# Kernel tuning notes

Measured on AMD Instinct MI355X. Metric: run time of the kernel, lower is better.

The kernel has to match this reference:

```python
import jax, jax.numpy as jnp
import numpy as np

B, L, D = 4, 4096, 1024
LN_EPS = 1e-5
SCAN_EPS = 1e-8


def setup_inputs() -> dict:
    key = jax.random.key(0)
    ks = jax.random.split(key, 5)
    s = 1.0 / np.sqrt(D)
    return {
        "X": jax.random.normal(ks[0], (B, L, D), dtype=jnp.float32),
        "Wa": jax.random.normal(ks[1], (D, D), dtype=jnp.float32) * s,
        "ba": jnp.zeros((D,), dtype=jnp.float32),
        "Wb": jax.random.normal(ks[2], (D, D), dtype=jnp.float32) * s,
        "bb": jnp.zeros((D,), dtype=jnp.float32),
        "Wc": jax.random.normal(ks[3], (D, D), dtype=jnp.float32) * s,
        "bc": jnp.zeros((D,), dtype=jnp.float32),
        "gamma": jnp.ones((D,), dtype=jnp.float32),
        "beta": jnp.zeros((D,), dtype=jnp.float32),
        "h0": jax.random.normal(ks[4], (1, D), dtype=jnp.float32),
    }


def reference(X, Wa, ba, Wb, bb, Wc, bc, gamma, beta, h0):
    # LayerNorm over last dim
    mu = jnp.mean(X, axis=-1, keepdims=True)
    var = jnp.mean(jnp.square(X - mu), axis=-1, keepdims=True)
    Z = (X - mu) * jax.lax.rsqrt(var + LN_EPS) * gamma + beta  # [B,L,D]

    A = jax.nn.sigmoid(jnp.einsum("bld,ed->ble", Z, Wa) + ba)   # gate in (0,1)
    P = jnp.cumprod(A, axis=1)                                   # decay products
    Bx = jnp.einsum("bld,ed->ble", Z, Wb) + bb
    S = jnp.cumsum(Bx / (P + SCAN_EPS), axis=1)
    # h_t = P_t * h0 + P_t * sum_{s<=t} Bx_s / P_s   (linear recurrence)
    h = P * (h0[:, None, :] + S)                                 # h0 [1,D] broadcasts
    C = jnp.einsum("bld,ed->ble", Z, Wc) + bc
    return C * h + X  # dropout is identity at inference
```

## Files before the change

kernel.cpp:

```cpp
#include <hip/hip_runtime.h>
#include <hip/hip_bf16.h>
#include <cstdint>
#include <cstddef>

#define B_ 4
#define L_ 4096
#define D_ 1024
#define M_ (B_ * L_)
#define LN_EPS 1e-5f
#define SCAN_EPS 1e-8f
#define CT 64
#define NC (L_ / CT)

typedef float f32x4 __attribute__((ext_vector_type(4)));
typedef short bf16x8 __attribute__((ext_vector_type(8)));

__device__ __forceinline__ void gload_lds16(const void* g, void* l) {
    __builtin_amdgcn_global_load_lds(
        (const __attribute__((address_space(1))) void*)g,
        (__attribute__((address_space(3))) void*)l, 16, 0, 0);
}

__global__ __launch_bounds__(256) void ln_kernel(
    const float* __restrict__ X, const float* __restrict__ gamma,
    const float* __restrict__ beta, __hip_bfloat16* __restrict__ Zb)
{
    const int row = blockIdx.x;
    const int tid = threadIdx.x;
    const float* x = X + (size_t)row * D_;

    float4 v = *reinterpret_cast<const float4*>(x + tid * 4);
    float s = v.x + v.y + v.z + v.w;
    #pragma unroll
    for (int off = 32; off > 0; off >>= 1) s += __shfl_down(s, off);

    __shared__ float red[4];
    __shared__ float red2[4];
    const int wid = tid >> 6, lane = tid & 63;
    if (lane == 0) red[wid] = s;
    __syncthreads();
    const float mean = (red[0] + red[1] + red[2] + red[3]) * (1.0f / D_);

    const float dx = v.x - mean, dy = v.y - mean, dz = v.z - mean, dw = v.w - mean;
    float s2 = dx * dx + dy * dy + dz * dz + dw * dw;
    #pragma unroll
    for (int off = 32; off > 0; off >>= 1) s2 += __shfl_down(s2, off);
    if (lane == 0) red2[wid] = s2;
    __syncthreads();
    const float var = (red2[0] + red2[1] + red2[2] + red2[3]) * (1.0f / D_);
    const float rs = rsqrtf(var + LN_EPS);

    float4 g  = *reinterpret_cast<const float4*>(gamma + tid * 4);
    float4 be = *reinterpret_cast<const float4*>(beta + tid * 4);
    union { ushort4 u4; __hip_bfloat16 h[4]; } pk;
    pk.h[0] = __float2bfloat16(dx * rs * g.x + be.x);
    pk.h[1] = __float2bfloat16(dy * rs * g.y + be.y);
    pk.h[2] = __float2bfloat16(dz * rs * g.z + be.z);
    pk.h[3] = __float2bfloat16(dw * rs * g.w + be.w);
    *reinterpret_cast<ushort4*>(Zb + (size_t)row * D_ + tid * 4) = pk.u4;
}

__global__ __launch_bounds__(256) void cvt_w3(
    const float* __restrict__ Wa, const float* __restrict__ Wb,
    const float* __restrict__ Wc, __hip_bfloat16* __restrict__ Wbf)
{
    const int gid = blockIdx.x * 256 + threadIdx.x;
    const size_t i = (size_t)gid * 8;
    const int which = (int)(i >> 20);
    const size_t off = i & ((1ull << 20) - 1);
    const float* W = (which == 0) ? Wa : (which == 1) ? Wb : Wc;
    float4 v0 = *reinterpret_cast<const float4*>(W + off);
    float4 v1 = *reinterpret_cast<const float4*>(W + off + 4);
    union { bf16x8 v; __hip_bfloat16 h[8]; } pk;
    pk.h[0] = __float2bfloat16(v0.x); pk.h[1] = __float2bfloat16(v0.y);
    pk.h[2] = __float2bfloat16(v0.z); pk.h[3] = __float2bfloat16(v0.w);
    pk.h[4] = __float2bfloat16(v1.x); pk.h[5] = __float2bfloat16(v1.y);
    pk.h[6] = __float2bfloat16(v1.z); pk.h[7] = __float2bfloat16(v1.w);
    *reinterpret_cast<bf16x8*>(Wbf + i) = pk.v;
}

#define TM 128
#define TN 128
#define TK 32

__global__ __launch_bounds__(256) void gemm3_mfma(
    const __hip_bfloat16* __restrict__ Zb, const __hip_bfloat16* __restrict__ Wbf,
    const float* __restrict__ ba, const float* __restrict__ bb, const float* __restrict__ bc,
    float* __restrict__ Aout, float* __restrict__ Bxout, float* __restrict__ Cout)
{
    __shared__ __hip_bfloat16 As[TM * TK];
    __shared__ __hip_bfloat16 Bs[TN * TK];

    const int tid  = threadIdx.x;
    const int wv   = tid >> 6;
    const int lane = tid & 63;
    const int wr   = wv >> 1, wc = wv & 1;
    const int m0   = blockIdx.y * TM;
    const int n0g  = blockIdx.x * TN;
    const int which = n0g >> 10;
    const int n0   = n0g & 1023;

    const __hip_bfloat16* __restrict__ Wsrc = Wbf + ((size_t)which << 20);
    const float* __restrict__ bias = (which == 0) ? ba : (which == 1) ? bb : bc;

    const int c0 = tid, c1 = 256 + tid;
    const int row0 = c0 >> 2, sc0 = (c0 & 3) ^ ((row0 >> 1) & 3);
    const int row1 = c1 >> 2, sc1 = (c1 & 3) ^ ((row1 >> 1) & 3);
    __hip_bfloat16* aDst0 = As + (size_t)(wv * 64) * 8;
    __hip_bfloat16* aDst1 = As + (size_t)(256 + wv * 64) * 8;
    __hip_bfloat16* bDst0 = Bs + (size_t)(wv * 64) * 8;
    __hip_bfloat16* bDst1 = Bs + (size_t)(256 + wv * 64) * 8;

    f32x4 acc[4][4] = {};

    for (int k0 = 0; k0 < D_; k0 += TK) {
        __syncthreads();
        gload_lds16(Zb   + (size_t)(m0 + row0) * D_ + k0 + sc0 * 8, aDst0);
        gload_lds16(Zb   + (size_t)(m0 + row1) * D_ + k0 + sc1 * 8, aDst1);
        gload_lds16(Wsrc + (size_t)(n0 + row0) * D_ + k0 + sc0 * 8, bDst0);
        gload_lds16(Wsrc + (size_t)(n0 + row1) * D_ + k0 + sc1 * 8, bDst1);
        __syncthreads();

        bf16x8 af[4], bfr[4];
        const int rl = lane & 15, kg = lane >> 4;
        #pragma unroll
        for (int i = 0; i < 4; ++i) {
            const int ra = wr * 64 + i * 16 + rl;
            af[i] = *reinterpret_cast<const bf16x8*>(
                reinterpret_cast<const char*>(As) + ra * 64 + ((kg ^ ((ra >> 1) & 3)) << 4));
            const int rb = wc * 64 + i * 16 + rl;
            bfr[i] = *reinterpret_cast<const bf16x8*>(
                reinterpret_cast<const char*>(Bs) + rb * 64 + ((kg ^ ((rb >> 1) & 3)) << 4));
        }
        #pragma unroll
        for (int i = 0; i < 4; ++i)
            #pragma unroll
            for (int j = 0; j < 4; ++j)
                acc[i][j] = __builtin_amdgcn_mfma_f32_16x16x32_bf16(
                    af[i], bfr[j], acc[i][j], 0, 0, 0);
    }

    float* __restrict__ Out = (which == 0) ? Aout : (which == 1) ? Bxout : Cout;
    const int cn = n0 + wc * 64 + (lane & 15);
    float bj[4];
    #pragma unroll
    for (int j = 0; j < 4; ++j) bj[j] = bias[cn + j * 16];

    #pragma unroll
    for (int i = 0; i < 4; ++i) {
        #pragma unroll
        for (int r = 0; r < 4; ++r) {
            const int m = m0 + wr * 64 + i * 16 + (lane >> 4) * 4 + r;
            float* dst = Out + (size_t)m * D_ + cn;
            #pragma unroll
            for (int j = 0; j < 4; ++j) {
                float val = acc[i][j][r] + bj[j];
                if (which == 0) val = 1.0f / (1.0f + expf(-val));
                dst[j * 16] = val;
            }
        }
    }
}

__global__ __launch_bounds__(256) void scan_chunkprod(
    const float* __restrict__ A, float* __restrict__ LP)
{
    const int id = blockIdx.x * 256 + threadIdx.x;
    const int e = id & (D_ - 1);
    const int c = (id >> 10) & (NC - 1);
    const int b = id >> 16;
    size_t base = ((size_t)b * L_ + (size_t)c * CT) * D_ + e;
    float p = 1.0f;
    #pragma unroll 8
    for (int t = 0; t < CT; ++t) p *= A[base + (size_t)t * D_];
    LP[id] = p;
}

__global__ __launch_bounds__(256) void scan_chunkpfx(
    const float* __restrict__ LP, float* __restrict__ Pstart)
{
    const int id = blockIdx.x * 256 + threadIdx.x;
    const int e = id & (D_ - 1);
    const int b = id >> 10;
    const size_t base = (size_t)b * NC * D_ + e;
    float p = 1.0f;
    for (int c = 0; c < NC; ++c) {
        Pstart[base + (size_t)c * D_] = p;
        p *= LP[base + (size_t)c * D_];
    }
}

__global__ __launch_bounds__(256) void scan_chunksum(
    const float* __restrict__ A, const float* __restrict__ Bx,
    const float* __restrict__ Pstart, float* __restrict__ Ssum)
{
    const int id = blockIdx.x * 256 + threadIdx.x;
    const int e = id & (D_ - 1);
    const int c = (id >> 10) & (NC - 1);
    const int b = id >> 16;
    size_t base = ((size_t)b * L_ + (size_t)c * CT) * D_ + e;
    float p = Pstart[id];
    float s = 0.0f;
    #pragma unroll 4
    for (int t = 0; t < CT; ++t) {
        const size_t idx = base + (size_t)t * D_;
        p *= A[idx];
        s += Bx[idx] / (p + SCAN_EPS);
    }
    Ssum[id] = s;
}

__global__ __launch_bounds__(256) void scan_sumpfx(
    const float* __restrict__ Ssum, float* __restrict__ Sstart)
{
    const int id = blockIdx.x * 256 + threadIdx.x;
    const int e = id & (D_ - 1);
    const int b = id >> 10;
    const size_t base = (size_t)b * NC * D_ + e;
    float s = 0.0f;
    for (int c = 0; c < NC; ++c) {
        Sstart[base + (size_t)c * D_] = s;
        s += Ssum[base + (size_t)c * D_];
    }
}

__global__ __launch_bounds__(256) void scan_final(
    const float* __restrict__ A, const float* __restrict__ Bx,
    const float* __restrict__ X,
    const float* __restrict__ Pstart, const float* __restrict__ Sstart,
    const float* __restrict__ h0, float* __restrict__ out)
{
    const int id = blockIdx.x * 256 + threadIdx.x;
    const int e = id & (D_ - 1);
    const int c = (id >> 10) & (NC - 1);
    const int b = id >> 16;
    size_t base = ((size_t)b * L_ + (size_t)c * CT) * D_ + e;
    float p = Pstart[id];
    float s = Sstart[id];
    const float h0e = h0[e];
    #pragma unroll 4
    for (int t = 0; t < CT; ++t) {
        const size_t idx = base + (size_t)t * D_;
        p *= A[idx];
        s += Bx[idx] / (p + SCAN_EPS);
        const float h = p * (h0e + s);
        out[idx] = fmaf(out[idx], h, X[idx]);
    }
}

extern "C" void kernel_launch(void* const* d_in, const int* in_sizes, int n_in,
                              void* d_out, int out_size, void* d_ws, size_t ws_size,
                              hipStream_t stream)
{
    const float* X     = (const float*)d_in[0];
    const float* Wa    = (const float*)d_in[1];
    const float* ba    = (const float*)d_in[2];
    const float* Wb    = (const float*)d_in[3];
    const float* bb    = (const float*)d_in[4];
    const float* Wc    = (const float*)d_in[5];
    const float* bc    = (const float*)d_in[6];
    const float* gamma = (const float*)d_in[7];
    const float* beta  = (const float*)d_in[8];
    const float* h0    = (const float*)d_in[9];
    float* out = (float*)d_out;

    const size_t NELT = (size_t)M_ * D_;
    const size_t NCH  = (size_t)B_ * NC * D_;

    __hip_bfloat16* Zb  = (__hip_bfloat16*)d_ws;
    __hip_bfloat16* Wbf = Zb + NELT;
    float* Aarr = (float*)(Wbf + 3ull * 1024 * 1024);
    float* Bxa  = Aarr + NELT;
    float* LP   = Bxa  + NELT;
    float* Pst  = LP   + NCH;
    float* Ssum = Pst  + NCH;
    float* Sst  = Ssum + NCH;
    (void)ws_size; (void)in_sizes; (void)n_in; (void)out_size;

    cvt_w3<<<1536, 256, 0, stream>>>(Wa, Wb, Wc, Wbf);
    ln_kernel<<<M_, 256, 0, stream>>>(X, gamma, beta, Zb);

    gemm3_mfma<<<dim3(3072 / TN, M_ / TM), 256, 0, stream>>>(
        Zb, Wbf, ba, bb, bc, Aarr, Bxa, out);

    scan_chunkprod<<<1024, 256, 0, stream>>>(Aarr, LP);
    scan_chunkpfx<<<16, 256, 0, stream>>>(LP, Pst);
    scan_chunksum<<<1024, 256, 0, stream>>>(Aarr, Bxa, Pst, Ssum);
    scan_sumpfx<<<16, 256, 0, stream>>>(Ssum, Sst);
    scan_final<<<1024, 256, 0, stream>>>(Aarr, Bxa, X, Pst, Sst, h0, out);
}
```

Measured before the change: 392.9 us.

## Store GEMM outputs in bf16 and fuse chunk decay products into GEMM epilogue

The GEMM epilogue now writes A, Bx and C as bf16 instead of fp32, roughly halving the intermediate traffic that the scan kernels read back. The sigmoid branch also computes per-64-row chunk products of the gate with cross-lane shuffles and writes them straight to LP, so the separate scan_chunkprod pass over A is removed. The chunk product is taken over the bf16-rounded gate values so it matches what the later scans consume. The risk is accuracy: bf16 rounding of the gates compounds through long cumulative products and the division by P.

Result: faster. 352.2 us (-10.4%).

```diff
diff --git a/kernel.cpp b/kernel.cpp
--- a/kernel.cpp
+++ b/kernel.cpp
@@ -86,7 +86,8 @@
 __global__ __launch_bounds__(256) void gemm3_mfma(
     const __hip_bfloat16* __restrict__ Zb, const __hip_bfloat16* __restrict__ Wbf,
     const float* __restrict__ ba, const float* __restrict__ bb, const float* __restrict__ bc,
-    float* __restrict__ Aout, float* __restrict__ Bxout, float* __restrict__ Cout)
+    __hip_bfloat16* __restrict__ Aout, __hip_bfloat16* __restrict__ Bxout,
+    __hip_bfloat16* __restrict__ Cout, float* __restrict__ LP)
 {
     __shared__ __hip_bfloat16 As[TM * TK];
     __shared__ __hip_bfloat16 Bs[TN * TK];
@@ -140,40 +141,52 @@
                     af[i], bfr[j], acc[i][j], 0, 0, 0);
     }
 
-    float* __restrict__ Out = (which == 0) ? Aout : (which == 1) ? Bxout : Cout;
     const int cn = n0 + wc * 64 + (lane & 15);
     float bj[4];
     #pragma unroll
     for (int j = 0; j < 4; ++j) bj[j] = bias[cn + j * 16];
 
-    #pragma unroll
-    for (int i = 0; i < 4; ++i) {
-        #pragma unroll
-        for (int r = 0; r < 4; ++r) {
-            const int m = m0 + wr * 64 + i * 16 + (lane >> 4) * 4 + r;
-            float* dst = Out + (size_t)m * D_ + cn;
+    if (which == 0) {
+        float pp[4] = {1.0f, 1.0f, 1.0f, 1.0f};
+        #pragma unroll
+        for (int i = 0; i < 4; ++i) {
             #pragma unroll
-            for (int j = 0; j < 4; ++j) {
-                float val = acc[i][j][r] + bj[j];
-                if (which == 0) val = 1.0f / (1.0f + expf(-val));
-                dst[j * 16] = val;
+            for (int r = 0; r < 4; ++r) {
+                const int m = m0 + wr * 64 + i * 16 + (lane >> 4) * 4 + r;
+                __hip_bfloat16* dst = Aout + (size_t)m * D_ + cn;
+                #pragma unroll
+                for (int j = 0; j < 4; ++j) {
+                    const float val = 1.0f / (1.0f + expf(-(acc[i][j][r] + bj[j])));
+                    const __hip_bfloat16 hb = __float2bfloat16(val);
+                    dst[j * 16] = hb;
+                    pp[j] *= __bfloat162float(hb);
+                }
             }
         }
-    }
-}
-
-__global__ __launch_bounds__(256) void scan_chunkprod(
-    const float* __restrict__ A, float* __restrict__ LP)
-{
-    const int id = blockIdx.x * 256 + threadIdx.x;
-    const int e = id & (D_ - 1);
-    const int c = (id >> 10) & (NC - 1);
-    const int b = id >> 16;
-    size_t base = ((size_t)b * L_ + (size_t)c * CT) * D_ + e;
-    float p = 1.0f;
-    #pragma unroll 8
-    for (int t = 0; t < CT; ++t) p *= A[base + (size_t)t * D_];
-    LP[id] = p;
+        #pragma unroll
+        for (int j = 0; j < 4; ++j) {
+            pp[j] *= __shfl_xor(pp[j], 16);
+            pp[j] *= __shfl_xor(pp[j], 32);
+        }
+        const int rl = lane & 15, kg = lane >> 4;
+        const float sel = (kg == 0) ? pp[0] : (kg == 1) ? pp[1] : (kg == 2) ? pp[2] : pp[3];
+        const int bseq = m0 >> 12;
+        const int cidx = ((m0 & 4095) >> 6) + wr;
+        LP[((size_t)bseq * NC + cidx) * D_ + n0 + wc * 64 + kg * 16 + rl] = sel;
+    } else {
+        __hip_bfloat16* __restrict__ Out = (which == 1) ? Bxout : Cout;
+        #pragma unroll
+        for (int i = 0; i < 4; ++i) {
+            #pragma unroll
+            for (int r = 0; r < 4; ++r) {
+                const int m = m0 + wr * 64 + i * 16 + (lane >> 4) * 4 + r;
+                __hip_bfloat16* dst = Out + (size_t)m * D_ + cn;
+                #pragma unroll
+                for (int j = 0; j < 4; ++j)
+                    dst[j * 16] = __float2bfloat16(acc[i][j][r] + bj[j]);
+            }
+        }
+    }
 }
 
 __global__ __launch_bounds__(256) void scan_chunkpfx(
@@ -191,7 +204,7 @@
 }
 
 __global__ __launch_bounds__(256) void scan_chunksum(
-    const float* __restrict__ A, const float* __restrict__ Bx,
+    const __hip_bfloat16* __restrict__ A, const __hip_bfloat16* __restrict__ Bx,
     const float* __restrict__ Pstart, float* __restrict__ Ssum)
 {
     const int id = blockIdx.x * 256 + threadIdx.x;
@@ -204,8 +217,8 @@
     #pragma unroll 4
     for (int t = 0; t < CT; ++t) {
         const size_t idx = base + (size_t)t * D_;
-        p *= A[idx];
-        s += Bx[idx] / (p + SCAN_EPS);
+        p *= __bfloat162float(A[idx]);
+        s += __bfloat162float(Bx[idx]) / (p + SCAN_EPS);
     }
     Ssum[id] = s;
 }
@@ -225,8 +238,8 @@
 }
 
 __global__ __launch_bounds__(256) void scan_final(
-    const float* __restrict__ A, const float* __restrict__ Bx,
-    const float* __restrict__ X,
+    const __hip_bfloat16* __restrict__ A, const __hip_bfloat16* __restrict__ Bx,
+    const __hip_bfloat16* __restrict__ C, const float* __restrict__ X,
     const float* __restrict__ Pstart, const float* __restrict__ Sstart,
     const float* __restrict__ h0, float* __restrict__ out)
 {
@@ -241,10 +254,10 @@
     #pragma unroll 4
     for (int t = 0; t < CT; ++t) {
         const size_t idx = base + (size_t)t * D_;
-        p *= A[idx];
-        s += Bx[idx] / (p + SCAN_EPS);
+        p *= __bfloat162float(A[idx]);
+        s += __bfloat162float(Bx[idx]) / (p + SCAN_EPS);
         const float h = p * (h0e + s);
-        out[idx] = fmaf(out[idx], h, X[idx]);
+        out[idx] = fmaf(__bfloat162float(C[idx]), h, X[idx]);
     }
 }
 
@@ -267,11 +280,12 @@
     const size_t NELT = (size_t)M_ * D_;
     const size_t NCH  = (size_t)B_ * NC * D_;
 
-    __hip_bfloat16* Zb  = (__hip_bfloat16*)d_ws;
-    __hip_bfloat16* Wbf = Zb + NELT;
-    float* Aarr = (float*)(Wbf + 3ull * 1024 * 1024);
-    float* Bxa  = Aarr + NELT;
-    float* LP   = Bxa  + NELT;
+    __hip_bfloat16* Zb   = (__hip_bfloat16*)d_ws;
+    __hip_bfloat16* Wbf  = Zb + NELT;
+    __hip_bfloat16* Abf  = Wbf + 3ull * 1024 * 1024;
+    __hip_bfloat16* Bxbf = Abf + NELT;
+    __hip_bfloat16* Cbf  = Bxbf + NELT;
+    float* LP   = (float*)(Cbf + NELT);
     float* Pst  = LP   + NCH;
     float* Ssum = Pst  + NCH;
     float* Sst  = Ssum + NCH;
@@ -281,11 +295,10 @@
     ln_kernel<<<M_, 256, 0, stream>>>(X, gamma, beta, Zb);
 
     gemm3_mfma<<<dim3(3072 / TN, M_ / TM), 256, 0, stream>>>(
-        Zb, Wbf, ba, bb, bc, Aarr, Bxa, out);
-
-    scan_chunkprod<<<1024, 256, 0, stream>>>(Aarr, LP);
+        Zb, Wbf, ba, bb, bc, Abf, Bxbf, Cbf, LP);
+
     scan_chunkpfx<<<16, 256, 0, stream>>>(LP, Pst);
-    scan_chunksum<<<1024, 256, 0, stream>>>(Aarr, Bxa, Pst, Ssum);
+    scan_chunksum<<<1024, 256, 0, stream>>>(Abf, Bxbf, Pst, Ssum);
     scan_sumpfx<<<16, 256, 0, stream>>>(Ssum, Sst);
-    scan_final<<<1024, 256, 0, stream>>>(Aarr, Bxa, X, Pst, Sst, h0, out);
-}
+    scan_final<<<1024, 256, 0, stream>>>(Abf, Bxbf, Cbf, X, Pst, Sst, h0, out);
+}
```
